# Optimization experiments

Hardware: AMD Instinct MI355X
Metric: run time of the kernel (lower is better)

## Reference

```python
import jax, jax.numpy as jnp
import numpy as np

SELECTED_NUM = 4096
BN_EPS = 1e-5


def _conv1d(x, w, pad):
    # x: [B, C_in, L], w: [C_out, C_in, K]
    return jax.lax.conv_general_dilated(
        x, w, window_strides=(1,), padding=[(pad, pad)],
        dimension_numbers=('NCH', 'OIH', 'NCH'))


def _bn(x, g, b, m, v):
    # eval-mode BatchNorm1d over channel dim of [B, C, L]
    inv = g / jnp.sqrt(v + BN_EPS)
    return x * inv[None, :, None] + (b - m * inv)[None, :, None]


def setup_inputs() -> dict:
    key = jax.random.key(0)
    ks = jax.random.split(key, 16)
    B, N, CODE, NCLS = 4, 262144, 7, 3
    inp = {
        'box_preds': jax.random.normal(ks[0], (B, N, CODE), jnp.float32),
        'cls_preds': jax.random.normal(ks[1], (B, N, NCLS), jnp.float32),
        # conv_share: Conv1d(10,32,3) + BN(32) + ReLU + Conv1d(32,64,3) + BN(64) + ReLU
        'conv1_w': jax.random.normal(ks[2], (32, 10, 3), jnp.float32) * 0.1,
        'bn1_g': jax.random.uniform(ks[3], (32,), jnp.float32, 0.5, 1.5),
        'bn1_b': jax.random.normal(ks[4], (32,), jnp.float32) * 0.1,
        'bn1_m': jax.random.normal(ks[5], (32,), jnp.float32) * 0.1,
        'bn1_v': jax.random.uniform(ks[6], (32,), jnp.float32, 0.5, 1.5),
        'conv2_w': jax.random.normal(ks[7], (64, 32, 3), jnp.float32) * 0.1,
        'bn2_g': jax.random.uniform(ks[8], (64,), jnp.float32, 0.5, 1.5),
        'bn2_b': jax.random.normal(ks[9], (64,), jnp.float32) * 0.1,
        'bn2_m': jax.random.normal(ks[10], (64,), jnp.float32) * 0.1,
        'bn2_v': jax.random.uniform(ks[11], (64,), jnp.float32, 0.5, 1.5),
        # heads: Conv1d(64,5,1,bias=True), Conv1d(64,1,1,bias=True)
        'bin_w': jax.random.normal(ks[12], (5, 64, 1), jnp.float32) * 0.1,
        'bin_b': jnp.full((5,), -float(np.log((1 - 0.01) / 0.01)), jnp.float32),
        'res_w': jax.random.normal(ks[13], (1, 64, 1), jnp.float32) * 0.001,
        'res_b': jnp.zeros((1,), jnp.float32),
    }
    return inp


def reference(box_preds, cls_preds, conv1_w, bn1_g, bn1_b, bn1_m, bn1_v,
              conv2_w, bn2_g, bn2_b, bn2_m, bn2_v, bin_w, bin_b, res_w, res_b):
    # ---- proposal_layer: per-batch sigmoid(max-cls-score) topk + gather ----
    score = jax.nn.sigmoid(jnp.max(cls_preds, axis=-1))          # [B, N]
    _, sel = jax.lax.top_k(score, SELECTED_NUM)                  # [B, K]
    box_sel = jnp.take_along_axis(box_preds, sel[:, :, None], axis=1)  # [B, K, 7]
    cls_sel = jnp.take_along_axis(cls_preds, sel[:, :, None], axis=1)  # [B, K, 3]

    # ---- conv_share + heads over channel-first layout [B, 10, K] ----
    x = jnp.concatenate([box_sel, cls_sel], axis=-1).transpose(0, 2, 1)  # [B, 10, K]
    x = jax.nn.relu(_bn(_conv1d(x, conv1_w, 1), bn1_g, bn1_b, bn1_m, bn1_v))
    x = jax.nn.relu(_bn(_conv1d(x, conv2_w, 1), bn2_g, bn2_b, bn2_m, bn2_v))  # [B, 64, K]

    iou_bin = _conv1d(x, bin_w, 0) + bin_b[None, :, None]        # [B, 5, K]
    iou_res = _conv1d(x, res_w, 0) + res_b[None, :, None]        # [B, 1, K]

    iou_preds_bin = iou_bin.transpose(0, 2, 1)                   # [B, K, 5]
    iou_preds_residual = iou_res.transpose(0, 2, 1)              # [B, K, 1]
    return iou_preds_bin, iou_preds_residual, box_sel, cls_sel
```

## Files before the change

kernel.cpp:

```cpp
#include <hip/hip_runtime.h>
#include <stdint.h>

#define NPTS 262144
#define NB 4
#define KSEL 4096
#define CAP 8192
#define SLICES 8
#define SLICE_LEN (CAP / SLICES)
#define CBLK 128
#define HBLK 64

#define OFF_BITS  0ULL
#define OFF_H8P   (4ULL*NPTS*NB)
#define OFF_H12   (OFF_H8P + 4ULL*256*HBLK*NB)
#define OFF_CTRL  (OFF_H12 + 4ULL*4096*NB)
#define OFF_GRANK (OFF_CTRL + 1024ULL)
#define OFF_CAND  (OFF_GRANK + 4ULL*CAP*NB)
#define WS_NEEDED (OFF_CAND + 8ULL*CAP*NB)

#define OBIN 0
#define ORES (NB*KSEL*5)
#define OBOX (ORES + NB*KSEL)
#define OCLS (OBOX + NB*KSEL*7)


__device__ __forceinline__ uint32_t key_of(float mx) {
    uint32_t b = __float_as_uint(mx);
    uint32_t mask = ((int32_t)b >> 31) | 0x80000000u;
    return b ^ mask;
}

__global__ __launch_bounds__(256) void k_score_hist(
    const float* __restrict__ cls, uint32_t* __restrict__ bits, uint32_t* __restrict__ h8p)
{
    __shared__ uint32_t lh[8][256];
    for (int i = threadIdx.x; i < 2048; i += 256) ((uint32_t*)lh)[i] = 0;
    __syncthreads();
    int b = blockIdx.y;
    int sub = threadIdx.x >> 5;
    for (int it = 0; it < 4; ++it) {
        int chunk = blockIdx.x * 1024 + it * 256 + threadIdx.x;
        const float4* p = (const float4*)(cls + ((size_t)b * NPTS + (size_t)chunk * 4) * 3);
        float4 v0 = p[0], v1 = p[1], v2 = p[2];
        uint4 o;
        o.x = key_of(fmaxf(fmaxf(v0.x, v0.y), v0.z));
        o.y = key_of(fmaxf(fmaxf(v0.w, v1.x), v1.y));
        o.z = key_of(fmaxf(fmaxf(v1.z, v1.w), v2.x));
        o.w = key_of(fmaxf(fmaxf(v2.y, v2.z), v2.w));
        ((uint4*)(bits + (size_t)b * NPTS))[chunk] = o;
        atomicAdd(&lh[sub][o.x >> 24], 1u);
        atomicAdd(&lh[sub][o.y >> 24], 1u);
        atomicAdd(&lh[sub][o.z >> 24], 1u);
        atomicAdd(&lh[sub][o.w >> 24], 1u);
    }
    __syncthreads();
    uint32_t c = 0;
    #pragma unroll
    for (int s = 0; s < 8; ++s) c += lh[s][threadIdx.x];
    h8p[((size_t)b * HBLK + blockIdx.x) * 256 + threadIdx.x] = c;
}

__global__ __launch_bounds__(256) void k_scan8(
    const uint32_t* __restrict__ h8p, uint32_t* __restrict__ ctrl,
    uint32_t* __restrict__ h12, uint32_t* __restrict__ grank)
{
    __shared__ uint32_t s[256];
    int b = blockIdx.x;
    uint32_t sum = 0;
    const uint32_t* base = h8p + (size_t)b * HBLK * 256 + threadIdx.x;
    #pragma unroll 8
    for (int blk = 0; blk < HBLK; ++blk) sum += base[blk * 256];
    s[threadIdx.x] = sum;
    uint4* z = (uint4*)(h12 + (size_t)b * 4096);
    #pragma unroll
    for (int i = 0; i < 4; ++i) z[threadIdx.x + i * 256] = make_uint4(0u, 0u, 0u, 0u);
    uint4* zg = (uint4*)(grank + (size_t)b * CAP);
    #pragma unroll
    for (int i = 0; i < 8; ++i) zg[threadIdx.x + i * 256] = make_uint4(0u, 0u, 0u, 0u);
    __syncthreads();
    if (threadIdx.x == 0) {
        ctrl[b * 16 + 3] = 0u;
        uint32_t running = 0;
        for (int i = 255; i >= 0; --i) {
            if (running + s[i] >= (uint32_t)KSEL) {
                ctrl[b * 16 + 0] = (uint32_t)i;
                ctrl[b * 16 + 1] = running;
                break;
            }
            running += s[i];
        }
    }
}

__global__ __launch_bounds__(256) void k_hist12(
    const uint32_t* __restrict__ bits, const uint32_t* __restrict__ ctrl, uint32_t* __restrict__ h12)
{
    __shared__ uint32_t lh[4096];
    for (int i = threadIdx.x; i < 4096; i += 256) lh[i] = 0;
    __syncthreads();
    int b = blockIdx.y;
    uint32_t P8 = ctrl[b * 16 + 0];
    for (int it = 0; it < 4; ++it) {
        int chunk = blockIdx.x * 1024 + it * 256 + threadIdx.x;
        uint4 v = ((const uint4*)(bits + (size_t)b * NPTS))[chunk];
        if ((v.x >> 24) == P8) atomicAdd(&lh[(v.x >> 12) & 0xFFFu], 1u);
        if ((v.y >> 24) == P8) atomicAdd(&lh[(v.y >> 12) & 0xFFFu], 1u);
        if ((v.z >> 24) == P8) atomicAdd(&lh[(v.z >> 12) & 0xFFFu], 1u);
        if ((v.w >> 24) == P8) atomicAdd(&lh[(v.w >> 12) & 0xFFFu], 1u);
    }
    __syncthreads();
    for (int i = threadIdx.x; i < 4096; i += 256) {
        uint32_t c = lh[i];
        if (c) atomicAdd(&h12[(size_t)b * 4096 + i], c);
    }
}

__global__ __launch_bounds__(256) void k_scan12(
    const uint32_t* __restrict__ h12, uint32_t* __restrict__ ctrl)
{
    __shared__ uint32_t bins[4096];
    __shared__ uint32_t part[256];
    int b = blockIdx.x;
    const uint4* src = (const uint4*)(h12 + (size_t)b * 4096);
    for (int i = threadIdx.x; i < 1024; i += 256)
        ((uint4*)bins)[i] = src[i];
    __syncthreads();
    uint32_t s = 0;
    int base = threadIdx.x * 16;
    #pragma unroll
    for (int j = 0; j < 16; ++j) s += bins[base + j];
    part[threadIdx.x] = s;
    __syncthreads();
    if (threadIdx.x == 0) {
        uint32_t K = (uint32_t)KSEL - ctrl[b * 16 + 1];
        uint32_t running = 0; int seg = 0;
        for (int t = 255; t >= 0; --t) {
            if (running + part[t] >= K) { seg = t; break; }
            running += part[t];
        }
        for (int i = 15; i >= 0; --i) {
            running += bins[seg * 16 + i];
            if (running >= K) {
                ctrl[b * 16 + 2] = (ctrl[b * 16 + 0] << 12) | (uint32_t)(seg * 16 + i);
                break;
            }
        }
    }
}

__global__ __launch_bounds__(256) void k_compact(
    const uint32_t* __restrict__ bits, uint32_t* __restrict__ ctrl, uint64_t* __restrict__ cand)
{
    __shared__ uint32_t wbase[4];
    int b = blockIdx.y;
    uint32_t T = ctrl[b * 16 + 2];
    int lane = threadIdx.x & 63;
    int wave = threadIdx.x >> 6;
    uint64_t lmask = (1ull << lane) - 1ull;

    int chunk0 = blockIdx.x * 512 + threadIdx.x;
    const uint4* src = (const uint4*)(bits + (size_t)b * NPTS);
    uint4 v0 = src[chunk0];
    uint4 v1 = src[chunk0 + 256];
    uint32_t ks[8] = {v0.x, v0.y, v0.z, v0.w, v1.x, v1.y, v1.z, v1.w};
    bool sel[8];
    #pragma unroll
    for (int i = 0; i < 8; ++i) sel[i] = (ks[i] >> 12) >= T;

    uint32_t wsum = 0;
    #pragma unroll
    for (int i = 0; i < 8; ++i) wsum += (uint32_t)__popcll(__ballot(sel[i]));
    if (lane == 0) wbase[wave] = wsum;
    __syncthreads();
    if (threadIdx.x == 0) {
        uint32_t c0 = wbase[0], c1 = wbase[1], c2 = wbase[2], c3 = wbase[3];
        uint32_t tot = c0 + c1 + c2 + c3;
        uint32_t base = tot ? atomicAdd(&ctrl[b * 16 + 3], tot) : 0u;
        wbase[0] = base;
        wbase[1] = base + c0;
        wbase[2] = base + c0 + c1;
        wbase[3] = base + c0 + c1 + c2;
    }
    __syncthreads();
    uint32_t off = wbase[wave];
    #pragma unroll
    for (int i = 0; i < 8; ++i) {
        uint64_t m = __ballot(sel[i]);
        if (sel[i]) {
            uint32_t pos = off + (uint32_t)__popcll(m & lmask);
            uint32_t n = (uint32_t)(chunk0 + (i < 4 ? 0 : 256)) * 4 + (uint32_t)(i & 3);
            if (pos < CAP)
                cand[(size_t)b * CAP + pos] = ((uint64_t)(~ks[i]) << 32) | (uint64_t)n;
        }
        off += (uint32_t)__popcll(m);
    }
}

__global__ __launch_bounds__(256) void k_rank1(
    const uint64_t* __restrict__ cand, const uint32_t* __restrict__ ctrl,
    uint32_t* __restrict__ grank)
{
    __shared__ uint64_t keys[SLICE_LEN];
    int b = blockIdx.z;
    uint32_t C = ctrl[b * 16 + 3];
    if (C > CAP) C = CAP;
    uint32_t k0 = blockIdx.y * SLICE_LEN;
    if (k0 >= C) return;
    uint32_t nk = C - k0; if (nk > SLICE_LEN) nk = SLICE_LEN;
    for (uint32_t i = threadIdx.x; i < nk; i += 256)
        keys[i] = cand[(size_t)b * CAP + k0 + i];
    __syncthreads();
    uint32_t item = blockIdx.x * 256 + threadIdx.x;
    if (item >= C) return;
    uint64_t me = cand[(size_t)b * CAP + item];
    uint32_t r = 0;
    #pragma unroll 16
    for (uint32_t i = 0; i < nk; ++i) r += (keys[i] < me) ? 1u : 0u;
    atomicAdd(&grank[b * CAP + item], r);
}

__global__ __launch_bounds__(256) void k_rank2(
    const uint64_t* __restrict__ cand, const uint32_t* __restrict__ ctrl,
    const uint32_t* __restrict__ grank,
    const float* __restrict__ box, const float* __restrict__ cls, float* __restrict__ out)
{
    int b = blockIdx.y;
    uint32_t C = ctrl[b * 16 + 3];
    if (C > CAP) C = CAP;
    uint32_t item = blockIdx.x * 256 + threadIdx.x;
    if (item >= C) return;
    uint64_t me = cand[(size_t)b * CAP + item];
    uint32_t rank = grank[b * CAP + item];
    if (rank < KSEL) {
        uint32_t n = (uint32_t)me;
        const float* bp = box + ((size_t)b * NPTS + n) * 7;
        float* ob = out + OBOX + ((size_t)b * KSEL + rank) * 7;
        #pragma unroll
        for (int c = 0; c < 7; ++c) ob[c] = bp[c];
        const float* cp = cls + ((size_t)b * NPTS + n) * 3;
        float* oc = out + OCLS + ((size_t)b * KSEL + rank) * 3;
        #pragma unroll
        for (int c = 0; c < 3; ++c) oc[c] = cp[c];
    }
}

__global__ __launch_bounds__(256) void k_conv(
    const float* __restrict__ c1w, const float* __restrict__ g1v, const float* __restrict__ b1v,
    const float* __restrict__ m1v, const float* __restrict__ v1v,
    const float* __restrict__ c2w, const float* __restrict__ g2v, const float* __restrict__ b2v,
    const float* __restrict__ m2v, const float* __restrict__ v2v,
    const float* __restrict__ binw, const float* __restrict__ binb,
    const float* __restrict__ resw, const float* __restrict__ resb,
    float* __restrict__ out)
{
    __shared__ __align__(16) float w1s[960];
    __shared__ __align__(16) float b1s[32];
    __shared__ __align__(16) float w2s[6144];
    __shared__ __align__(16) float b2s[64];
    __shared__ __align__(16) float hws[6][64];
    __shared__ __align__(16) float xin[10][80];
    __shared__ __align__(16) float x1s[32][68];
    __shared__ __align__(16) float x2t[64][68];

    int tid = threadIdx.x;
    int b = blockIdx.y;
    int tile0 = blockIdx.x * 64;
    const float* boxsel = out + OBOX + (size_t)b * KSEL * 7;
    const float* clssel = out + OCLS + (size_t)b * KSEL * 3;

    for (int t = tid; t < 960; t += 256) {
        int c = t / 30, r = t - c * 30, i = r / 3, tap = r - i * 3;
        float inv = g1v[c] * rsqrtf(v1v[c] + 1e-5f);
        w1s[(i * 3 + tap) * 32 + c] = c1w[t] * inv;
    }
    if (tid < 32) {
        float inv = g1v[tid] * rsqrtf(v1v[tid] + 1e-5f);
        b1s[tid] = b1v[tid] - m1v[tid] * inv;
    }
    for (int t = tid; t < 6144; t += 256) {
        int o = t / 96, r = t - o * 96, i = r / 3, tap = r - i * 3;
        float inv = g2v[o] * rsqrtf(v2v[o] + 1e-5f);
        w2s[(i * 3 + tap) * 64 + o] = c2w[t] * inv;
    }
    if (tid >= 64 && tid < 128) {
        int o = tid - 64;
        float inv = g2v[o] * rsqrtf(v2v[o] + 1e-5f);
        b2s[o] = b2v[o] - m2v[o] * inv;
    }
    for (int t = tid; t < 384; t += 256)
        ((float*)hws)[t] = (t < 320) ? binw[t] : resw[t - 320];

    for (int u = tid; u < 680; u += 256) {
        int c = u / 68, k2 = u - c * 68;
        int g = tile0 + k2 - 2;
        float val = 0.f;
        if (g >= 0 && g < KSEL) val = (c < 7) ? boxsel[g * 7 + c] : clssel[g * 3 + (c - 7)];
        xin[c][k2] = val;
    }
    __syncthreads();

    {
        int c = tid & 31, kg = tid >> 5;
        int k0 = kg * 9;
        int nk = 66 - k0; if (nk > 9) nk = 9;
        float a[9];
        #pragma unroll
        for (int kk = 0; kk < 9; ++kk) a[kk] = b1s[c];
        #pragma unroll 2
        for (int i = 0; i < 10; ++i) {
            float xv[11];
            #pragma unroll
            for (int j = 0; j < 11; ++j) xv[j] = xin[i][k0 + j];
            #pragma unroll
            for (int tap = 0; tap < 3; ++tap) {
                float w = w1s[(i * 3 + tap) * 32 + c];
                #pragma unroll
                for (int kk = 0; kk < 9; ++kk) a[kk] = fmaf(w, xv[kk + tap], a[kk]);
            }
        }
        for (int kk = 0; kk < nk; ++kk) {
            int k = k0 + kk, gp = tile0 + k - 1;
            x1s[c][k] = (gp >= 0 && gp < KSEL) ? fmaxf(a[kk], 0.f) : 0.f;
        }
    }
    __syncthreads();

    {
        int o = tid & 63, pg = tid >> 6;
        int p0 = pg * 16;
        float acc[16];
        float bz = b2s[o];
        #pragma unroll
        for (int kk = 0; kk < 16; ++kk) acc[kk] = bz;
        #pragma unroll 4
        for (int i = 0; i < 32; ++i) {
            float4 xq[5];
            const float4* xr = (const float4*)&x1s[i][p0];
            #pragma unroll
            for (int q = 0; q < 5; ++q) xq[q] = xr[q];
            const float* xf = (const float*)xq;
            float w0 = w2s[(i * 3 + 0) * 64 + o];
            float w1 = w2s[(i * 3 + 1) * 64 + o];
            float w2 = w2s[(i * 3 + 2) * 64 + o];
            #pragma unroll
            for (int kk = 0; kk < 16; ++kk) {
                float t0 = fmaf(w0, xf[kk], acc[kk]);
                t0 = fmaf(w1, xf[kk + 1], t0);
                acc[kk] = fmaf(w2, xf[kk + 2], t0);
            }
        }
        #pragma unroll
        for (int kk = 0; kk < 16; ++kk)
            x2t[p0 + kk][o] = fmaxf(acc[kk], 0.f);
    }
    __syncthreads();

    {
        int p = tid & 63, g = tid >> 6;
        const float4* xr = (const float4*)&x2t[p][0];
        const float4* hw4 = (const float4*)hws;
        size_t gpos = (size_t)b * KSEL + (size_t)(tile0 + p);
        if (g < 2) {
            int j0 = g * 2, j1 = j0 + 1;
            float s0 = 0.f, s1 = 0.f;
            #pragma unroll
            for (int q = 0; q < 16; ++q) {
                float4 xv = xr[q];
                float4 wa = hw4[j0 * 16 + q];
                float4 wb = hw4[j1 * 16 + q];
                s0 = fmaf(xv.x, wa.x, s0); s0 = fmaf(xv.y, wa.y, s0);
                s0 = fmaf(xv.z, wa.z, s0); s0 = fmaf(xv.w, wa.w, s0);
                s1 = fmaf(xv.x, wb.x, s1); s1 = fmaf(xv.y, wb.y, s1);
                s1 = fmaf(xv.z, wb.z, s1); s1 = fmaf(xv.w, wb.w, s1);
            }
            out[OBIN + gpos * 5 + j0] = s0 + binb[j0];
            out[OBIN + gpos * 5 + j1] = s1 + binb[j1];
        } else {
            int j = (g == 2) ? 4 : 5;
            float s = 0.f;
            #pragma unroll
            for (int q = 0; q < 16; ++q) {
                float4 xv = xr[q];
                float4 wa = hw4[j * 16 + q];
                s = fmaf(xv.x, wa.x, s); s = fmaf(xv.y, wa.y, s);
                s = fmaf(xv.z, wa.z, s); s = fmaf(xv.w, wa.w, s);
            }
            if (g == 2) out[OBIN + gpos * 5 + 4] = s + binb[4];
            else        out[ORES + gpos]         = s + resb[0];
        }
    }
}

extern "C" void kernel_launch(void* const* d_in, const int* in_sizes, int n_in,
                              void* d_out, int out_size, void* d_ws, size_t ws_size,
                              hipStream_t stream)
{
    const float* box  = (const float*)d_in[0];
    const float* cls  = (const float*)d_in[1];
    const float* c1w  = (const float*)d_in[2];
    const float* g1   = (const float*)d_in[3];
    const float* b1   = (const float*)d_in[4];
    const float* m1   = (const float*)d_in[5];
    const float* v1   = (const float*)d_in[6];
    const float* c2w  = (const float*)d_in[7];
    const float* g2   = (const float*)d_in[8];
    const float* b2   = (const float*)d_in[9];
    const float* m2   = (const float*)d_in[10];
    const float* v2   = (const float*)d_in[11];
    const float* binw = (const float*)d_in[12];
    const float* binb = (const float*)d_in[13];
    const float* resw = (const float*)d_in[14];
    const float* resb = (const float*)d_in[15];
    float* out = (float*)d_out;
    char* ws = (char*)d_ws;
    if (ws_size < WS_NEEDED) return;

    uint32_t* bits  = (uint32_t*)(ws + OFF_BITS);
    uint32_t* h8p   = (uint32_t*)(ws + OFF_H8P);
    uint32_t* h12   = (uint32_t*)(ws + OFF_H12);
    uint32_t* ctrl  = (uint32_t*)(ws + OFF_CTRL);
    uint32_t* grank = (uint32_t*)(ws + OFF_GRANK);
    uint64_t* cand  = (uint64_t*)(ws + OFF_CAND);

    k_score_hist<<<dim3(HBLK, NB), 256, 0, stream>>>(cls, bits, h8p);
    k_scan8<<<NB, 256, 0, stream>>>(h8p, ctrl, h12, grank);
    k_hist12<<<dim3(HBLK, NB), 256, 0, stream>>>(bits, ctrl, h12);
    k_scan12<<<NB, 256, 0, stream>>>(h12, ctrl);
    k_compact<<<dim3(CBLK, NB), 256, 0, stream>>>(bits, ctrl, cand);
    k_rank1<<<dim3(CAP / 256, SLICES, NB), 256, 0, stream>>>(cand, ctrl, grank);
    k_rank2<<<dim3(CAP / 256, NB), 256, 0, stream>>>(cand, ctrl, grank, box, cls, out);
    k_conv<<<dim3(64, NB), 256, 0, stream>>>(c1w, g1, b1, m1, v1, c2w, g2, b2, m2, v2,
                                             binw, binb, resw, resb, out);
}
```

Measured before the change: 83.64 us.

## Fold scan kernels into histogram and compact kernels, register-block rank pass

Removes the two single-block scan kernels. Each block of the 12-bit histogram and compaction kernels now redundantly recomputes the prefix search over the histogram, and the zeroing of h12, grank and the counter moves into the score histogram kernel. The rank kernel now gives each thread four candidates against 1024-key shared slices, which reduces shared-memory loads and block count per comparison. The goal is fewer launches and serialization points, paid for with duplicated scan work in every block.

```diff
diff --git a/kernel.cpp b/kernel.cpp
--- a/kernel.cpp
+++ b/kernel.cpp
@@ -5,8 +5,7 @@
 #define NB 4
 #define KSEL 4096
 #define CAP 8192
-#define SLICES 8
-#define SLICE_LEN (CAP / SLICES)
+#define SLICE_LEN 1024
 #define CBLK 128
 #define HBLK 64
 
@@ -31,15 +30,16 @@
 }
 
 __global__ __launch_bounds__(256) void k_score_hist(
-    const float* __restrict__ cls, uint32_t* __restrict__ bits, uint32_t* __restrict__ h8p)
+    const float* __restrict__ cls, uint32_t* __restrict__ bits, uint32_t* __restrict__ h8p,
+    uint32_t* __restrict__ h12, uint32_t* __restrict__ grank, uint32_t* __restrict__ ctrl)
 {
     __shared__ uint32_t lh[8][256];
     for (int i = threadIdx.x; i < 2048; i += 256) ((uint32_t*)lh)[i] = 0;
     __syncthreads();
-    int b = blockIdx.y;
+    int b = blockIdx.y, bx = blockIdx.x;
     int sub = threadIdx.x >> 5;
     for (int it = 0; it < 4; ++it) {
-        int chunk = blockIdx.x * 1024 + it * 256 + threadIdx.x;
+        int chunk = bx * 1024 + it * 256 + threadIdx.x;
         const float4* p = (const float4*)(cls + ((size_t)b * NPTS + (size_t)chunk * 4) * 3);
         float4 v0 = p[0], v1 = p[1], v2 = p[2];
         uint4 o;
@@ -53,55 +53,54 @@
         atomicAdd(&lh[sub][o.z >> 24], 1u);
         atomicAdd(&lh[sub][o.w >> 24], 1u);
     }
+    if (bx == 1) {
+        uint4* z = (uint4*)(h12 + (size_t)b * 4096);
+        #pragma unroll
+        for (int i = 0; i < 4; ++i) z[threadIdx.x + i * 256] = make_uint4(0u, 0u, 0u, 0u);
+    } else if (bx == 2) {
+        uint4* zg = (uint4*)(grank + (size_t)b * CAP);
+        #pragma unroll
+        for (int i = 0; i < 8; ++i) zg[threadIdx.x + i * 256] = make_uint4(0u, 0u, 0u, 0u);
+    } else if (bx == 3 && threadIdx.x == 0) {
+        ctrl[b * 16 + 3] = 0u;
+    }
     __syncthreads();
     uint32_t c = 0;
     #pragma unroll
     for (int s = 0; s < 8; ++s) c += lh[s][threadIdx.x];
-    h8p[((size_t)b * HBLK + blockIdx.x) * 256 + threadIdx.x] = c;
-}
-
-__global__ __launch_bounds__(256) void k_scan8(
-    const uint32_t* __restrict__ h8p, uint32_t* __restrict__ ctrl,
-    uint32_t* __restrict__ h12, uint32_t* __restrict__ grank)
-{
-    __shared__ uint32_t s[256];
-    int b = blockIdx.x;
+    h8p[((size_t)b * HBLK + bx) * 256 + threadIdx.x] = c;
+}
+
+__global__ __launch_bounds__(256) void k_hist12(
+    const uint32_t* __restrict__ bits, const uint32_t* __restrict__ h8p,
+    uint32_t* __restrict__ ctrl, uint32_t* __restrict__ h12)
+{
+    __shared__ uint32_t lh[4096];
+    __shared__ uint32_t part[256];
+    __shared__ uint32_t P8s;
+    int b = blockIdx.y, bx = blockIdx.x;
+    for (int i = threadIdx.x; i < 4096; i += 256) lh[i] = 0;
     uint32_t sum = 0;
-    const uint32_t* base = h8p + (size_t)b * HBLK * 256 + threadIdx.x;
+    const uint32_t* hp = h8p + (size_t)b * HBLK * 256 + threadIdx.x;
     #pragma unroll 8
-    for (int blk = 0; blk < HBLK; ++blk) sum += base[blk * 256];
-    s[threadIdx.x] = sum;
-    uint4* z = (uint4*)(h12 + (size_t)b * 4096);
-    #pragma unroll
-    for (int i = 0; i < 4; ++i) z[threadIdx.x + i * 256] = make_uint4(0u, 0u, 0u, 0u);
-    uint4* zg = (uint4*)(grank + (size_t)b * CAP);
-    #pragma unroll
-    for (int i = 0; i < 8; ++i) zg[threadIdx.x + i * 256] = make_uint4(0u, 0u, 0u, 0u);
+    for (int blk = 0; blk < HBLK; ++blk) sum += hp[blk * 256];
+    part[threadIdx.x] = sum;
     __syncthreads();
     if (threadIdx.x == 0) {
-        ctrl[b * 16 + 3] = 0u;
         uint32_t running = 0;
         for (int i = 255; i >= 0; --i) {
-            if (running + s[i] >= (uint32_t)KSEL) {
-                ctrl[b * 16 + 0] = (uint32_t)i;
-                ctrl[b * 16 + 1] = running;
+            if (running + part[i] >= (uint32_t)KSEL) {
+                P8s = (uint32_t)i;
+                if (bx == 0) { ctrl[b * 16 + 0] = (uint32_t)i; ctrl[b * 16 + 1] = running; }
                 break;
             }
-            running += s[i];
-        }
-    }
-}
-
-__global__ __launch_bounds__(256) void k_hist12(
-    const uint32_t* __restrict__ bits, const uint32_t* __restrict__ ctrl, uint32_t* __restrict__ h12)
-{
-    __shared__ uint32_t lh[4096];
-    for (int i = threadIdx.x; i < 4096; i += 256) lh[i] = 0;
-    __syncthreads();
-    int b = blockIdx.y;
-    uint32_t P8 = ctrl[b * 16 + 0];
+            running += part[i];
+        }
+    }
+    __syncthreads();
+    const uint32_t P8 = P8s;
     for (int it = 0; it < 4; ++it) {
-        int chunk = blockIdx.x * 1024 + it * 256 + threadIdx.x;
+        int chunk = bx * 1024 + it * 256 + threadIdx.x;
         uint4 v = ((const uint4*)(bits + (size_t)b * NPTS))[chunk];
         if ((v.x >> 24) == P8) atomicAdd(&lh[(v.x >> 12) & 0xFFFu], 1u);
         if ((v.y >> 24) == P8) atomicAdd(&lh[(v.y >> 12) & 0xFFFu], 1u);
@@ -115,23 +114,28 @@
     }
 }
 
-__global__ __launch_bounds__(256) void k_scan12(
-    const uint32_t* __restrict__ h12, uint32_t* __restrict__ ctrl)
+__global__ __launch_bounds__(256) void k_compact(
+    const uint32_t* __restrict__ bits, const uint32_t* __restrict__ h12,
+    uint32_t* __restrict__ ctrl, uint64_t* __restrict__ cand)
 {
     __shared__ uint32_t bins[4096];
     __shared__ uint32_t part[256];
-    int b = blockIdx.x;
+    __shared__ uint32_t Ts;
+    __shared__ uint32_t wbase[4];
+    int b = blockIdx.y, bx = blockIdx.x;
     const uint4* src = (const uint4*)(h12 + (size_t)b * 4096);
-    for (int i = threadIdx.x; i < 1024; i += 256)
-        ((uint4*)bins)[i] = src[i];
-    __syncthreads();
-    uint32_t s = 0;
-    int base = threadIdx.x * 16;
-    #pragma unroll
-    for (int j = 0; j < 16; ++j) s += bins[base + j];
-    part[threadIdx.x] = s;
+    for (int i = threadIdx.x; i < 1024; i += 256) ((uint4*)bins)[i] = src[i];
+    __syncthreads();
+    {
+        uint32_t s = 0;
+        int base2 = threadIdx.x * 16;
+        #pragma unroll
+        for (int j = 0; j < 16; ++j) s += bins[base2 + j];
+        part[threadIdx.x] = s;
+    }
     __syncthreads();
     if (threadIdx.x == 0) {
+        uint32_t P8 = ctrl[b * 16 + 0];
         uint32_t K = (uint32_t)KSEL - ctrl[b * 16 + 1];
         uint32_t running = 0; int seg = 0;
         for (int t = 255; t >= 0; --t) {
@@ -140,28 +144,18 @@
         }
         for (int i = 15; i >= 0; --i) {
             running += bins[seg * 16 + i];
-            if (running >= K) {
-                ctrl[b * 16 + 2] = (ctrl[b * 16 + 0] << 12) | (uint32_t)(seg * 16 + i);
-                break;
-            }
-        }
-    }
-}
-
-__global__ __launch_bounds__(256) void k_compact(
-    const uint32_t* __restrict__ bits, uint32_t* __restrict__ ctrl, uint64_t* __restrict__ cand)
-{
-    __shared__ uint32_t wbase[4];
-    int b = blockIdx.y;
-    uint32_t T = ctrl[b * 16 + 2];
-    int lane = threadIdx.x & 63;
-    int wave = threadIdx.x >> 6;
-    uint64_t lmask = (1ull << lane) - 1ull;
-
-    int chunk0 = blockIdx.x * 512 + threadIdx.x;
-    const uint4* src = (const uint4*)(bits + (size_t)b * NPTS);
-    uint4 v0 = src[chunk0];
-    uint4 v1 = src[chunk0 + 256];
+            if (running >= K) { Ts = (P8 << 12) | (uint32_t)(seg * 16 + i); break; }
+        }
+    }
+    __syncthreads();
+    const uint32_t T = Ts;
+    const int lane = threadIdx.x & 63, wave = threadIdx.x >> 6;
+    const uint64_t lmask = (1ull << lane) - 1ull;
+
+    int chunk0 = bx * 512 + threadIdx.x;
+    const uint4* sb = (const uint4*)(bits + (size_t)b * NPTS);
+    uint4 v0 = sb[chunk0];
+    uint4 v1 = sb[chunk0 + 256];
     uint32_t ks[8] = {v0.x, v0.y, v0.z, v0.w, v1.x, v1.y, v1.z, v1.w};
     bool sel[8];
     #pragma unroll
@@ -204,19 +198,31 @@
     int b = blockIdx.z;
     uint32_t C = ctrl[b * 16 + 3];
     if (C > CAP) C = CAP;
-    uint32_t k0 = blockIdx.y * SLICE_LEN;
-    if (k0 >= C) return;
-    uint32_t nk = C - k0; if (nk > SLICE_LEN) nk = SLICE_LEN;
-    for (uint32_t i = threadIdx.x; i < nk; i += 256)
-        keys[i] = cand[(size_t)b * CAP + k0 + i];
-    __syncthreads();
-    uint32_t item = blockIdx.x * 256 + threadIdx.x;
-    if (item >= C) return;
-    uint64_t me = cand[(size_t)b * CAP + item];
-    uint32_t r = 0;
-    #pragma unroll 16
-    for (uint32_t i = 0; i < nk; ++i) r += (keys[i] < me) ? 1u : 0u;
-    atomicAdd(&grank[b * CAP + item], r);
+    uint32_t ig0 = blockIdx.x * 1024;
+    uint32_t sk0 = blockIdx.y * SLICE_LEN;
+    if (ig0 >= C || sk0 >= C) return;
+    uint32_t nk = C - sk0; if (nk > SLICE_LEN) nk = SLICE_LEN;
+    const uint64_t* cb = cand + (size_t)b * CAP;
+    for (uint32_t i = threadIdx.x; i < nk; i += 256) keys[i] = cb[sk0 + i];
+    __syncthreads();
+    uint64_t me[4];
+    uint32_t idx[4], r[4] = {0u, 0u, 0u, 0u};
+    #pragma unroll
+    for (int q = 0; q < 4; ++q) {
+        idx[q] = ig0 + (uint32_t)q * 256 + threadIdx.x;
+        me[q] = (idx[q] < C) ? cb[idx[q]] : ~0ull;
+    }
+    #pragma unroll 8
+    for (uint32_t i = 0; i < nk; ++i) {
+        uint64_t k = keys[i];
+        r[0] += (k < me[0]) ? 1u : 0u;
+        r[1] += (k < me[1]) ? 1u : 0u;
+        r[2] += (k < me[2]) ? 1u : 0u;
+        r[3] += (k < me[3]) ? 1u : 0u;
+    }
+    #pragma unroll
+    for (int q = 0; q < 4; ++q)
+        if (idx[q] < C) atomicAdd(&grank[b * CAP + idx[q]], r[q]);
 }
 
 __global__ __launch_bounds__(256) void k_rank2(
@@ -228,6 +234,7 @@
     uint32_t C = ctrl[b * 16 + 3];
     if (C > CAP) C = CAP;
     uint32_t item = blockIdx.x * 256 + threadIdx.x;
+    if (blockIdx.x * 256 >= C) return;
     if (item >= C) return;
     uint64_t me = cand[(size_t)b * CAP + item];
     uint32_t rank = grank[b * CAP + item];
@@ -422,12 +429,10 @@
     uint32_t* grank = (uint32_t*)(ws + OFF_GRANK);
     uint64_t* cand  = (uint64_t*)(ws + OFF_CAND);
 
-    k_score_hist<<<dim3(HBLK, NB), 256, 0, stream>>>(cls, bits, h8p);
-    k_scan8<<<NB, 256, 0, stream>>>(h8p, ctrl, h12, grank);
-    k_hist12<<<dim3(HBLK, NB), 256, 0, stream>>>(bits, ctrl, h12);
-    k_scan12<<<NB, 256, 0, stream>>>(h12, ctrl);
-    k_compact<<<dim3(CBLK, NB), 256, 0, stream>>>(bits, ctrl, cand);
-    k_rank1<<<dim3(CAP / 256, SLICES, NB), 256, 0, stream>>>(cand, ctrl, grank);
+    k_score_hist<<<dim3(HBLK, NB), 256, 0, stream>>>(cls, bits, h8p, h12, grank, ctrl);
+    k_hist12<<<dim3(HBLK, NB), 256, 0, stream>>>(bits, h8p, ctrl, h12);
+    k_compact<<<dim3(CBLK, NB), 256, 0, stream>>>(bits, h12, ctrl, cand);
+    k_rank1<<<dim3(CAP / 1024, CAP / 1024, NB), 256, 0, stream>>>(cand, ctrl, grank);
     k_rank2<<<dim3(CAP / 256, NB), 256, 0, stream>>>(cand, ctrl, grank, box, cls, out);
     k_conv<<<dim3(64, NB), 256, 0, stream>>>(c1w, g1, b1, m1, v1, c2w, g2, b2, m2, v2,
                                              binw, binb, resw, resb, out);
```

Result: slower. 87.27 us (+4.3%).
